# Performance work log

Measured on AMD Instinct MI355X. Metric: run time of the kernel, lower is better.

## Reference

```python
import jax, jax.numpy as jnp
import numpy as np

PAD = 7                 # init padding
T = 2 * PAD + 1         # T_side_dense = 15 shifts per axis
LAMDA = 1.0             # init lamda
EPS = 1e-16             # hardcoded epsilon in the torch loss body


def _joint_hist(x_out, x_tf_out):
    # Equivalent of F.conv2d(x_out.permute(1,0,2,3), weight=x_tf_out.permute(1,0,2,3), padding=PAD)
    # expressed as T*T shifted matmuls (correlation / cost-volume form).
    bn, k, h, w = x_out.shape
    A = jnp.transpose(x_out, (1, 0, 2, 3))      # (k, bn, h, w)  conv "input"
    B = jnp.transpose(x_tf_out, (1, 0, 2, 3))   # (k, bn, h, w)  conv "weight"
    A_pad = jnp.pad(A, ((0, 0), (0, 0), (PAD, PAD), (PAD, PAD)))

    def step(carry, s):
        dy, dx = s // T, s % T
        sl = jax.lax.dynamic_slice(A_pad, (0, 0, dy, dx), (k, bn, h, w))
        # p[n, o] at this shift = sum_{c,y,x} A_pad[n,c,y+dy,x+dx] * B[o,c,y,x]
        return carry, jnp.einsum('nchw,ochw->no', sl, B)

    _, p = jax.lax.scan(step, None, jnp.arange(T * T))
    # (T*T, k, k) -> (T, T, k, k); matches torch p_i_j.permute(2, 3, 0, 1)
    return p.reshape(T, T, k, k)


def reference(x_out, x_tf_out):
    p = _joint_hist(x_out, x_tf_out)
    # shift to positive; min is detached in torch -> stop_gradient
    p = p - jax.lax.stop_gradient(p.min()) + EPS
    # normalize per shift over the (k, k) joint
    p = p / p.sum(axis=(2, 3), keepdims=True)
    # symmetrize
    p = (p + jnp.swapaxes(p, 2, 3)) / 2.0
    p_i = p.sum(axis=2, keepdims=True)   # (T, T, 1, k) marginal (broadcasts like repeat)
    p_j = p.sum(axis=3, keepdims=True)   # (T, T, k, 1) marginal
    loss = (-p * (jnp.log(p + EPS)
                  - LAMDA * jnp.log(p_i + EPS)
                  - LAMDA * jnp.log(p_j + EPS))).sum() / (T * T)
    return loss


def setup_inputs() -> dict:
    key = jax.random.key(0)
    k1, k2 = jax.random.split(key)
    bn, k, h, w = 16, 10, 224, 224
    # simplex over axis=1 is asserted by the torch module -> use softmax
    x_out = jax.nn.softmax(jax.random.normal(k1, (bn, k, h, w), dtype=jnp.float32), axis=1)
    x_tf_out = jax.nn.softmax(jax.random.normal(k2, (bn, k, h, w), dtype=jnp.float32), axis=1)
    return {"x_out": x_out, "x_tf_out": x_tf_out}
```

## Files before the change

### kernel.cpp

```cpp
#include <hip/hip_runtime.h>
#include <stdint.h>
#include <math.h>


#define PADV 7
#define TS 15
#define KCLS 10
#define HH 224
#define WW 224
#define MD 160
#define NCELL (MD*MD)
#define NBLK 512
#define TY 7
#define AROW 240
#define BSTRIDE 232
#define BPH 240
#define LEPS 1e-16

typedef __attribute__((ext_vector_type(4))) float f32x4;
typedef __attribute__((ext_vector_type(8))) short bf16x8;

__device__ __forceinline__ unsigned short f2bf(float f) {
  union { float f; uint32_t u; } v; v.f = f;
  return (unsigned short)((v.u + 0x7FFFu + ((v.u >> 16) & 1u)) >> 16);
}

__device__ __forceinline__ void glds16(const unsigned short* g, unsigned short* l) {
  __builtin_amdgcn_global_load_lds(
      (const __attribute__((address_space(1))) unsigned int*)g,
      (__attribute__((address_space(3))) unsigned int*)l, 16, 0, 0);
}

__global__ __launch_bounds__(256)
void prep_b(const float* __restrict__ xt, unsigned short* __restrict__ bp) {
  const int idx   = blockIdx.x * 256 + threadIdx.x;
  const int rowid = idx / 29;
  const int chunk = idx - rowid * 29;
  const int x0    = chunk * 8;
  const int yy    = rowid % BPH;
  const int cls   = rowid / BPH;
  const int row   = yy - PADV;
  union { unsigned short h[8]; uint4 v; } out;
  if (row >= 0 && row < HH && x0 < WW) {
    const float* src = xt + ((size_t)cls * HH + row) * WW + x0;
#pragma unroll
    for (int j = 0; j < 8; ++j) out.h[j] = f2bf(src[j]);
  } else {
    out.v = make_uint4(0u, 0u, 0u, 0u);
  }
  *(uint4*)(bp + (size_t)rowid * BSTRIDE + x0) = out.v;
}

__global__ __launch_bounds__(256, 2)
void corr_gemm(const float* __restrict__ xo, const unsigned short* __restrict__ bpad,
               float* __restrict__ partials) {
  __shared__ __align__(16) unsigned short ldsA[KCLS * AROW];
  __shared__ __align__(16) unsigned short ldsB[KCLS * 16 * BSTRIDE];

  const int tid  = threadIdx.x;
  const int bid  = blockIdx.x;
  const int b    = bid >> 5;
  const int y0   = (bid & 31) * TY;

  const int lane = tid & 63;
  const int wv   = tid >> 6;
  const int wm   = wv & 1;
  const int wn   = wv >> 1;
  const int quad = lane >> 4;
  const int l15  = lane & 15;

  f32x4 acc[5][5];
#pragma unroll
  for (int i = 0; i < 5; ++i)
#pragma unroll
    for (int j = 0; j < 5; ++j) acc[i][j] = (f32x4){0.f, 0.f, 0.f, 0.f};

  const float* Ab = xo + (size_t)b * KCLS * HH * WW;
  const unsigned short* Bb = bpad + (size_t)b * KCLS * BPH * BSTRIDE;

  for (int pr = wv; pr < 15 * KCLS; pr += 4) {
    const int r15  = pr / KCLS;
    const int o    = pr - r15 * KCLS;
    const int yy   = y0 + r15;
    const int slot = (y0 - PADV + r15) & 15;
    if (lane < 29)
      glds16(Bb + ((size_t)o * BPH + yy) * BSTRIDE + lane * 8,
             ldsB + (o * 16 + slot) * BSTRIDE);
  }

#pragma unroll
  for (int r = 0; r < 10; ++r) {
    const int t = tid + r * 256;
    if (t < KCLS * AROW) {
      const int n = t / AROW;
      const int i = t - n * AROW;
      const int x = i - PADV;
      float v = 0.f;
      if (x >= 0 && x < WW) v = Ab[((size_t)n * HH + y0) * WW + x];
      ldsA[t] = f2bf(v);
    }
  }
  __syncthreads();

  float va[10];
  for (int y = y0; y < y0 + TY; ++y) {
    const bool more = (y + 1 < y0 + TY);

    if (more) {
      const int yy   = y + 8 + PADV;
      const int slot = (y + 8) & 15;
      for (int ro = wv; ro < KCLS; ro += 4) {
        if (lane < 29)
          glds16(Bb + ((size_t)ro * BPH + yy) * BSTRIDE + lane * 8,
                 ldsB + (ro * 16 + slot) * BSTRIDE);
      }
      const int yl = y + 1;
#pragma unroll
      for (int r = 0; r < 10; ++r) {
        const int t = tid + r * 256;
        float v = 0.f;
        if (t < KCLS * AROW) {
          const int n = t / AROW;
          const int i = t - n * AROW;
          const int x = i - PADV;
          if (x >= 0 && x < WW) v = Ab[((size_t)n * HH + yl) * WW + x];
        }
        va[r] = v;
      }
    }

#pragma unroll 1
    for (int xc = 0; xc < 7; ++xc) {
      const int x0 = xc * 32;
      bf16x8 afrag[5], bfrag[5];
      const int e0 = x0 + quad * 8 + l15;
      const int q  = e0 >> 1;
      const int sh = (e0 & 1) << 4;
#pragma unroll
      for (int mi = 0; mi < 5; ++mi) {
        const int tm = wm * 5 + mi;
        const uint32_t* pa = (const uint32_t*)ldsA + tm * (AROW / 2);
        uint32_t w0 = pa[q], w1 = pa[q + 1], w2 = pa[q + 2],
                 w3 = pa[q + 3], w4 = pa[q + 4];
        union { uint32_t u[4]; bf16x8 v; } cv;
        cv.u[0] = __builtin_amdgcn_alignbit(w1, w0, sh);
        cv.u[1] = __builtin_amdgcn_alignbit(w2, w1, sh);
        cv.u[2] = __builtin_amdgcn_alignbit(w3, w2, sh);
        cv.u[3] = __builtin_amdgcn_alignbit(w4, w3, sh);
        afrag[mi] = cv.v;
      }
      const int slot = (y + PADV - l15) & 15;
#pragma unroll
      for (int ni = 0; ni < 5; ++ni) {
        const int to = wn * 5 + ni;
        bfrag[ni] = *(const bf16x8*)(ldsB + (to * 16 + slot) * BSTRIDE + x0 + quad * 8);
      }
#pragma unroll
      for (int mi = 0; mi < 5; ++mi)
#pragma unroll
        for (int ni = 0; ni < 5; ++ni)
          acc[mi][ni] = __builtin_amdgcn_mfma_f32_16x16x32_bf16(
              afrag[mi], bfrag[ni], acc[mi][ni], 0, 0, 0);
    }

    if (more) {
      __syncthreads();
#pragma unroll
      for (int r = 0; r < 10; ++r) {
        const int t = tid + r * 256;
        if (t < KCLS * AROW) ldsA[t] = f2bf(va[r]);
      }
      __syncthreads();
    }
  }

  float* outp = partials + (size_t)bid * NCELL;
#pragma unroll
  for (int mi = 0; mi < 5; ++mi)
#pragma unroll
    for (int ni = 0; ni < 5; ++ni) {
      const int mrow = (wm * 5 + mi) * 16 + quad * 4;
      const int ncol = (wn * 5 + ni) * 16 + l15;
#pragma unroll
      for (int r = 0; r < 4; ++r)
        outp[(size_t)(mrow + r) * MD + ncol] = acc[mi][ni][r];
    }
}

__global__ __launch_bounds__(256)
void reduce_stage1(const float* __restrict__ partials, float* __restrict__ stage2) {
  const int c  = (blockIdx.x % 100) * 256 + threadIdx.x;
  const int pg = blockIdx.x / 100;
  const float* base = partials + (size_t)pg * 64 * NCELL + c;
  float s0 = 0.f, s1 = 0.f, s2 = 0.f, s3 = 0.f;
  for (int p = 0; p < 64; p += 4) {
    s0 += base[(size_t)(p + 0) * NCELL];
    s1 += base[(size_t)(p + 1) * NCELL];
    s2 += base[(size_t)(p + 2) * NCELL];
    s3 += base[(size_t)(p + 3) * NCELL];
  }
  stage2[(size_t)pg * NCELL + c] = (s0 + s1) + (s2 + s3);
}

__global__ __launch_bounds__(256)
void reduce_final(const float* __restrict__ stage2, float* __restrict__ Cout,
                  float* __restrict__ mins, float* __restrict__ dout) {
  const int c = blockIdx.x * 256 + threadIdx.x;
  if (blockIdx.x == 0 && threadIdx.x == 0) dout[0] = 0.f;
  double s = 0.0;
#pragma unroll
  for (int pg = 0; pg < 8; ++pg) s += (double)stage2[(size_t)pg * NCELL + c];
  const float sf = (float)s;
  Cout[c] = sf;
  const int m  = c / MD;
  const int nn = c - m * MD;
  const bool valid = ((m & 15) < TS) && ((nn & 15) < TS);
  __shared__ float red[256];
  red[threadIdx.x] = valid ? sf : 3.4e38f;
  __syncthreads();
  for (int st = 128; st > 0; st >>= 1) {
    if (threadIdx.x < st)
      red[threadIdx.x] = fminf(red[threadIdx.x], red[threadIdx.x + st]);
    __syncthreads();
  }
  if (threadIdx.x == 0) mins[blockIdx.x] = red[0];
}

__global__ __launch_bounds__(128)
void loss_kernel(const float* __restrict__ Cmat, const float* __restrict__ mins,
                 float* __restrict__ dout) {
  const int s   = blockIdx.x;
  const int dy  = s / TS;
  const int dx  = s - dy * TS;
  const int tid = threadIdx.x;
  __shared__ float fm[128];
  __shared__ double q[100];
  __shared__ double sym[100];
  __shared__ double pi[10], pj[10];
  __shared__ double red[128];

  fm[tid] = (tid < 100) ? mins[tid] : 3.4e38f;
  __syncthreads();
  for (int st = 64; st > 0; st >>= 1) {
    if (tid < st) fm[tid] = fminf(fm[tid], fm[tid + st]);
    __syncthreads();
  }
  const double minv = (double)fm[0];
  __syncthreads();

  if (tid < 100) {
    const int n = tid / 10, o = tid - (tid / 10) * 10;
    const double v = (double)Cmat[(size_t)(n * 16 + dx) * MD + (o * 16 + dy)];
    q[tid] = v - minv + LEPS;
  }
  __syncthreads();
  red[tid] = (tid < 100) ? q[tid] : 0.0;
  __syncthreads();
  for (int st = 64; st > 0; st >>= 1) {
    if (tid < st) red[tid] += red[tid + st];
    __syncthreads();
  }
  const double Z = red[0];
  __syncthreads();
  if (tid < 100) {
    const int n = tid / 10, o = tid - (tid / 10) * 10;
    sym[tid] = (q[n * 10 + o] + q[o * 10 + n]) * 0.5 / Z;
  }
  __syncthreads();
  if (tid < 10) {
    double a = 0.0, bsum = 0.0;
    for (int n2 = 0; n2 < 10; ++n2) {
      a    += sym[n2 * 10 + tid];
      bsum += sym[tid * 10 + n2];
    }
    pi[tid] = a;
    pj[tid] = bsum;
  }
  __syncthreads();
  double term = 0.0;
  if (tid < 100) {
    const int n = tid / 10, o = tid - (tid / 10) * 10;
    const double sp = sym[tid];
    term = -sp * (log(sp + LEPS) - log(pi[o] + LEPS) - log(pj[n] + LEPS));
  }
  red[tid] = term;
  __syncthreads();
  for (int st = 64; st > 0; st >>= 1) {
    if (tid < st) red[tid] += red[tid + st];
    __syncthreads();
  }
  if (tid == 0) atomicAdd(dout, (float)(red[0] / (double)(TS * TS)));
}

extern "C" void kernel_launch(void* const* d_in, const int* in_sizes, int n_in,
                              void* d_out, int out_size, void* d_ws, size_t ws_size,
                              hipStream_t stream) {
  const float* xo = (const float*)d_in[0];
  const float* xt = (const float*)d_in[1];
  float* ws       = (float*)d_ws;

  float* partials = ws;
  float* stage2   = partials + (size_t)NBLK * NCELL;
  float* Cmat     = stage2 + (size_t)8 * NCELL;
  float* mins     = Cmat + NCELL;
  unsigned short* bpad = (unsigned short*)(mins + 128);
  float* out      = (float*)d_out;

  hipLaunchKernelGGL(prep_b,        dim3(4350), dim3(256), 0, stream, xt, bpad);
  hipLaunchKernelGGL(corr_gemm,     dim3(NBLK), dim3(256), 0, stream, xo, bpad, partials);
  hipLaunchKernelGGL(reduce_stage1, dim3(800),  dim3(256), 0, stream, partials, stage2);
  hipLaunchKernelGGL(reduce_final,  dim3(100),  dim3(256), 0, stream, stage2, Cmat, mins, out);
  hipLaunchKernelGGL(loss_kernel,   dim3(225),  dim3(128), 0, stream, Cmat, mins, out);
}
```

Before: 154.2 us.

## Use 640-thread blocks with 10 waves, double-buffered A rows, taller row tiles

The correlation GEMM now runs 256 blocks of 10 waves, each covering 14 image rows instead of 7. Each wave computes a 2x5 tile of 16x16 MFMA outputs instead of 5x5, which cuts accumulator registers and raises occupancy. The A row buffer in LDS is now double-buffered, which removes one barrier per row. Blocks are also remapped so consecutive block IDs spread across batches. Halving the block count also halves the partial-sum traffic into the reduction, at the cost of fewer blocks per CU and more wave-level LDS fragment reads.

```diff
diff --git a/kernel.cpp b/kernel.cpp
--- a/kernel.cpp
+++ b/kernel.cpp
@@ -10,8 +10,8 @@
 #define WW 224
 #define MD 160
 #define NCELL (MD*MD)
-#define NBLK 512
-#define TY 7
+#define NBLK 256
+#define TY 14
 #define AROW 240
 #define BSTRIDE 232
 #define BPH 240
@@ -51,34 +51,35 @@
   *(uint4*)(bp + (size_t)rowid * BSTRIDE + x0) = out.v;
 }
 
-__global__ __launch_bounds__(256, 2)
+__global__ __launch_bounds__(640, 3)
 void corr_gemm(const float* __restrict__ xo, const unsigned short* __restrict__ bpad,
                float* __restrict__ partials) {
-  __shared__ __align__(16) unsigned short ldsA[KCLS * AROW];
+  __shared__ __align__(16) unsigned short ldsA[2][KCLS * AROW];
   __shared__ __align__(16) unsigned short ldsB[KCLS * 16 * BSTRIDE];
 
   const int tid  = threadIdx.x;
-  const int bid  = blockIdx.x;
-  const int b    = bid >> 5;
-  const int y0   = (bid & 31) * TY;
+  const int bid0 = blockIdx.x;
+  const int bid  = (bid0 & 7) * 32 + (bid0 >> 3);
+  const int b    = bid >> 4;
+  const int y0   = (bid & 15) * TY;
 
   const int lane = tid & 63;
   const int wv   = tid >> 6;
-  const int wm   = wv & 1;
-  const int wn   = wv >> 1;
+  const int wm   = wv >> 1;
+  const int wn   = wv & 1;
   const int quad = lane >> 4;
   const int l15  = lane & 15;
 
-  f32x4 acc[5][5];
-#pragma unroll
-  for (int i = 0; i < 5; ++i)
+  f32x4 acc[2][5];
+#pragma unroll
+  for (int i = 0; i < 2; ++i)
 #pragma unroll
     for (int j = 0; j < 5; ++j) acc[i][j] = (f32x4){0.f, 0.f, 0.f, 0.f};
 
   const float* Ab = xo + (size_t)b * KCLS * HH * WW;
   const unsigned short* Bb = bpad + (size_t)b * KCLS * BPH * BSTRIDE;
 
-  for (int pr = wv; pr < 15 * KCLS; pr += 4) {
+  for (int pr = wv; pr < 15 * KCLS; pr += 10) {
     const int r15  = pr / KCLS;
     const int o    = pr - r15 * KCLS;
     const int yy   = y0 + r15;
@@ -89,35 +90,35 @@
   }
 
 #pragma unroll
-  for (int r = 0; r < 10; ++r) {
-    const int t = tid + r * 256;
+  for (int r = 0; r < 4; ++r) {
+    const int t = tid + r * 640;
     if (t < KCLS * AROW) {
       const int n = t / AROW;
       const int i = t - n * AROW;
       const int x = i - PADV;
       float v = 0.f;
       if (x >= 0 && x < WW) v = Ab[((size_t)n * HH + y0) * WW + x];
-      ldsA[t] = f2bf(v);
-    }
-  }
-  __syncthreads();
-
-  float va[10];
-  for (int y = y0; y < y0 + TY; ++y) {
-    const bool more = (y + 1 < y0 + TY);
+      ldsA[0][t] = f2bf(v);
+    }
+  }
+  __syncthreads();
+
+  int cur = 0;
+  float va[4];
+  for (int s = 0; s < TY; ++s) {
+    const int y = y0 + s;
+    const bool more = (s + 1 < TY);
 
     if (more) {
       const int yy   = y + 8 + PADV;
       const int slot = (y + 8) & 15;
-      for (int ro = wv; ro < KCLS; ro += 4) {
-        if (lane < 29)
-          glds16(Bb + ((size_t)ro * BPH + yy) * BSTRIDE + lane * 8,
-                 ldsB + (ro * 16 + slot) * BSTRIDE);
-      }
+      if (lane < 29)
+        glds16(Bb + ((size_t)wv * BPH + yy) * BSTRIDE + lane * 8,
+               ldsB + (wv * 16 + slot) * BSTRIDE);
       const int yl = y + 1;
 #pragma unroll
-      for (int r = 0; r < 10; ++r) {
-        const int t = tid + r * 256;
+      for (int r = 0; r < 4; ++r) {
+        const int t = tid + r * 640;
         float v = 0.f;
         if (t < KCLS * AROW) {
           const int n = t / AROW;
@@ -129,17 +130,18 @@
       }
     }
 
+    const unsigned short* la = ldsA[cur];
 #pragma unroll 1
     for (int xc = 0; xc < 7; ++xc) {
       const int x0 = xc * 32;
-      bf16x8 afrag[5], bfrag[5];
+      bf16x8 afrag[2], bfrag[5];
       const int e0 = x0 + quad * 8 + l15;
       const int q  = e0 >> 1;
       const int sh = (e0 & 1) << 4;
 #pragma unroll
-      for (int mi = 0; mi < 5; ++mi) {
-        const int tm = wm * 5 + mi;
-        const uint32_t* pa = (const uint32_t*)ldsA + tm * (AROW / 2);
+      for (int mi = 0; mi < 2; ++mi) {
+        const int tm = wm * 2 + mi;
+        const uint32_t* pa = (const uint32_t*)la + tm * (AROW / 2);
         uint32_t w0 = pa[q], w1 = pa[q + 1], w2 = pa[q + 2],
                  w3 = pa[q + 3], w4 = pa[q + 4];
         union { uint32_t u[4]; bf16x8 v; } cv;
@@ -156,7 +158,7 @@
         bfrag[ni] = *(const bf16x8*)(ldsB + (to * 16 + slot) * BSTRIDE + x0 + quad * 8);
       }
 #pragma unroll
-      for (int mi = 0; mi < 5; ++mi)
+      for (int mi = 0; mi < 2; ++mi)
 #pragma unroll
         for (int ni = 0; ni < 5; ++ni)
           acc[mi][ni] = __builtin_amdgcn_mfma_f32_16x16x32_bf16(
@@ -164,22 +166,23 @@
     }
 
     if (more) {
-      __syncthreads();
-#pragma unroll
-      for (int r = 0; r < 10; ++r) {
-        const int t = tid + r * 256;
-        if (t < KCLS * AROW) ldsA[t] = f2bf(va[r]);
+      unsigned short* an = ldsA[cur ^ 1];
+#pragma unroll
+      for (int r = 0; r < 4; ++r) {
+        const int t = tid + r * 640;
+        if (t < KCLS * AROW) an[t] = f2bf(va[r]);
       }
       __syncthreads();
+      cur ^= 1;
     }
   }
 
   float* outp = partials + (size_t)bid * NCELL;
 #pragma unroll
-  for (int mi = 0; mi < 5; ++mi)
+  for (int mi = 0; mi < 2; ++mi)
 #pragma unroll
     for (int ni = 0; ni < 5; ++ni) {
-      const int mrow = (wm * 5 + mi) * 16 + quad * 4;
+      const int mrow = (wm * 2 + mi) * 16 + quad * 4;
       const int ncol = (wn * 5 + ni) * 16 + l15;
 #pragma unroll
       for (int r = 0; r < 4; ++r)
@@ -191,9 +194,9 @@
 void reduce_stage1(const float* __restrict__ partials, float* __restrict__ stage2) {
   const int c  = (blockIdx.x % 100) * 256 + threadIdx.x;
   const int pg = blockIdx.x / 100;
-  const float* base = partials + (size_t)pg * 64 * NCELL + c;
+  const float* base = partials + (size_t)pg * 32 * NCELL + c;
   float s0 = 0.f, s1 = 0.f, s2 = 0.f, s3 = 0.f;
-  for (int p = 0; p < 64; p += 4) {
+  for (int p = 0; p < 32; p += 4) {
     s0 += base[(size_t)(p + 0) * NCELL];
     s1 += base[(size_t)(p + 1) * NCELL];
     s2 += base[(size_t)(p + 2) * NCELL];
@@ -307,7 +310,7 @@
   float* out      = (float*)d_out;
 
   hipLaunchKernelGGL(prep_b,        dim3(4350), dim3(256), 0, stream, xt, bpad);
-  hipLaunchKernelGGL(corr_gemm,     dim3(NBLK), dim3(256), 0, stream, xo, bpad, partials);
+  hipLaunchKernelGGL(corr_gemm,     dim3(NBLK), dim3(640), 0, stream, xo, bpad, partials);
   hipLaunchKernelGGL(reduce_stage1, dim3(800),  dim3(256), 0, stream, partials, stage2);
   hipLaunchKernelGGL(reduce_final,  dim3(100),  dim3(256), 0, stream, stage2, Cmat, mins, out);
   hipLaunchKernelGGL(loss_kernel,   dim3(225),  dim3(128), 0, stream, Cmat, mins, out);
```

Result: no change. 155.3 us (+0.7%).
